# Kernel optimization log

Measured on AMD Instinct MI355X. Metric: run time of the kernel, lower is better.

## Reference

```python
import jax, jax.numpy as jnp
import numpy as np

NUM_HEADS = 12
DIM = 768


def _ste_sign(x):
    # forward: sign with sign(0) = +1; backward: pass-through on |x| <= 1
    s = jnp.where(x >= 0, 1.0, -1.0).astype(x.dtype)
    base = jnp.clip(x, -1.0, 1.0)
    return base + jax.lax.stop_gradient(s - base)


def _quantize_qk(x):
    # s = mean(|x|) over last two dims (differentiable), times STE sign
    s = jnp.mean(jnp.abs(x), axis=(-2, -1), keepdims=True)
    return s * _ste_sign(x)


def _round_ste(z):
    return z + jax.lax.stop_gradient(jnp.round(z) - z)


def _quantize_p(x):
    qmax = 255.0
    s = 1.0 / qmax
    q = jnp.clip(_round_ste(x / s), 0.0, qmax)
    return s * q


def _quantize_v(x):
    # SymQuantizer fwd: per-column (dim=-2) absmax, detached; 8-bit symmetric
    m = jax.lax.stop_gradient(jnp.max(jnp.abs(x), axis=-2, keepdims=True))
    s = 127.0 / (m + 1e-6)
    qz = jnp.round(x * s) / (s + 1e-6)
    # backward STE: pass-through where -2 < x < 2 (clip_val = [-2, 2])
    base = jnp.clip(x, -2.0, 2.0)
    return base + jax.lax.stop_gradient(qz - base)


def _attention(x, w_qkv, w_proj, b_proj):
    B, C, H, W = x.shape
    N = H * W
    nh = NUM_HEADS
    hd = C // nh
    scale = hd ** (-0.5)
    xf = x.reshape(B, C, N).transpose(0, 2, 1)          # [B, N, C]
    qkv = xf @ w_qkv.T                                   # [B, N, 3C]
    qkv = qkv.reshape(B, N, 3, nh, hd).transpose(2, 0, 3, 1, 4)  # [3, B, h, N, d]
    q, k, v = qkv[0], qkv[1], qkv[2]
    q = _quantize_qk(q)
    k = _quantize_qk(k)
    attn = jnp.einsum('bhnd,bhmd->bhnm', q, k) * scale   # [B, h, N, N]
    attn = jax.nn.softmax(attn, axis=-1)
    attn = _quantize_p(attn)
    v = _quantize_v(v)
    out = jnp.einsum('bhnm,bhmd->bhnd', attn, v)         # [B, h, N, d]
    out = out.transpose(0, 2, 1, 3).reshape(B, N, C)
    out = out @ w_proj.T + b_proj                        # [B, N, C]
    return out.transpose(0, 2, 1).reshape(B, C, H, W)


def setup_inputs() -> dict:
    key = jax.random.key(0)
    k1, k2, k3, k4 = jax.random.split(key, 4)
    B, C, H, W = 16, DIM, 24, 24
    x = jax.random.normal(k1, (B, C, H, W), dtype=jnp.float32)
    w_qkv = jax.random.normal(k2, (3 * C, C), dtype=jnp.float32) * 0.02
    w_proj = jax.random.normal(k3, (C, C), dtype=jnp.float32) * 0.02
    b_proj = jax.random.normal(k4, (C,), dtype=jnp.float32) * 0.02
    return {"x": x, "w_qkv": w_qkv, "w_proj": w_proj, "b_proj": b_proj}


def reference(x, w_qkv, w_proj, b_proj):
    return _attention(x, w_qkv, w_proj, b_proj)
```

## Files before the change

kernel.cpp:

```cpp
#include <hip/hip_runtime.h>
#include <hip/hip_bf16.h>

#define B_   16
#define NH   12
#define NTOK 576
#define HD   64
#define CH   768
#define NELEM (B_*NH*NTOK*HD)
#define VT8STRIDE (NTOK*HD*4)

typedef short v8s __attribute__((ext_vector_type(8)));
typedef short v4s __attribute__((ext_vector_type(4)));
typedef float v4f __attribute__((ext_vector_type(4)));
typedef int   v4i __attribute__((ext_vector_type(4)));

static __device__ __forceinline__ void split4(const float* f, v4s& hi, v4s& lo)
{
    #pragma unroll
    for (int i = 0; i < 4; ++i) {
        __hip_bfloat16 h = __float2bfloat16(f[i]);
        float hf = __bfloat162float(h);
        __hip_bfloat16 l = __float2bfloat16(f[i] - hf);
        hi[i] = __builtin_bit_cast(short, h);
        lo[i] = __builtin_bit_cast(short, l);
    }
}

__global__ __launch_bounds__(256) void qkv_mfma(const float* __restrict__ x,
    const float* __restrict__ w, float* __restrict__ q, float* __restrict__ k,
    float* __restrict__ v)
{
    __shared__ short Ah[64*40], Al[64*40];
    __shared__ short Bh[256*40], Bl[256*40];
    const int tid = threadIdx.x;
    int g = blockIdx.x;
    g = (g & 7) * 162 + (g >> 3);
    const int b  = g / 81;
    const int rr = g % 81;
    const int jb = rr / 9;
    const int mb = rr % 9;
    const int n0 = mb * 64;
    const int j0 = jb * 256;
    const int lane = tid & 63, wv = tid >> 6;

    const int cq  = tid & 7;
    const int rw0 = tid >> 3;

    const float* xb  = x + (size_t)b * CH * NTOK + n0;
    const float* wbp = w + (size_t)j0 * CH;

    float areg[2][4];
    float breg[8][4];

    #pragma unroll
    for (int s = 0; s < 2; ++s) {
        const int nl = rw0 + 32*s;
        #pragma unroll
        for (int i = 0; i < 4; ++i)
            areg[s][i] = xb[(size_t)(cq*4 + i) * NTOK + nl];
    }
    #pragma unroll
    for (int s = 0; s < 8; ++s) {
        const int jl = rw0 + 32*s;
        const float4 t = *(const float4*)(wbp + (size_t)jl * CH + cq*4);
        breg[s][0]=t.x; breg[s][1]=t.y; breg[s][2]=t.z; breg[s][3]=t.w;
    }

    v4f acc[4][4];
    #pragma unroll
    for (int a = 0; a < 4; ++a)
        #pragma unroll
        for (int c = 0; c < 4; ++c) acc[a][c] = (v4f){0.f,0.f,0.f,0.f};

    for (int it = 0; it < 24; ++it) {
        __syncthreads();
        #pragma unroll
        for (int s = 0; s < 2; ++s) {
            v4s hi, lo; split4(areg[s], hi, lo);
            const int nl = rw0 + 32*s;
            *(v4s*)&Ah[nl*40 + cq*4] = hi;
            *(v4s*)&Al[nl*40 + cq*4] = lo;
        }
        #pragma unroll
        for (int s = 0; s < 8; ++s) {
            v4s hi, lo; split4(breg[s], hi, lo);
            const int jl = rw0 + 32*s;
            *(v4s*)&Bh[jl*40 + cq*4] = hi;
            *(v4s*)&Bl[jl*40 + cq*4] = lo;
        }
        __syncthreads();
        if (it < 23) {
            const int c0 = (it + 1) * 32;
            #pragma unroll
            for (int s = 0; s < 2; ++s) {
                const int nl = rw0 + 32*s;
                #pragma unroll
                for (int i = 0; i < 4; ++i)
                    areg[s][i] = xb[(size_t)(c0 + cq*4 + i) * NTOK + nl];
            }
            #pragma unroll
            for (int s = 0; s < 8; ++s) {
                const int jl = rw0 + 32*s;
                const float4 t = *(const float4*)(wbp + (size_t)jl * CH + c0 + cq*4);
                breg[s][0]=t.x; breg[s][1]=t.y; breg[s][2]=t.z; breg[s][3]=t.w;
            }
        }
        const int krow = lane & 15;
        const int k0   = (lane >> 4) * 8;
        v8s ah[4], al2[4], bh[4], bl[4];
        #pragma unroll
        for (int mt = 0; mt < 4; ++mt) {
            ah[mt]  = *(v8s*)&Ah[(mt*16 + krow)*40 + k0];
            al2[mt] = *(v8s*)&Al[(mt*16 + krow)*40 + k0];
        }
        #pragma unroll
        for (int jt = 0; jt < 4; ++jt) {
            bh[jt] = *(v8s*)&Bh[(wv*64 + jt*16 + krow)*40 + k0];
            bl[jt] = *(v8s*)&Bl[(wv*64 + jt*16 + krow)*40 + k0];
        }
        #pragma unroll
        for (int mt = 0; mt < 4; ++mt)
            #pragma unroll
            for (int jt = 0; jt < 4; ++jt) {
                acc[mt][jt] = __builtin_amdgcn_mfma_f32_16x16x32_bf16(ah[mt],  bh[jt], acc[mt][jt], 0, 0, 0);
                acc[mt][jt] = __builtin_amdgcn_mfma_f32_16x16x32_bf16(ah[mt],  bl[jt], acc[mt][jt], 0, 0, 0);
                acc[mt][jt] = __builtin_amdgcn_mfma_f32_16x16x32_bf16(al2[mt], bh[jt], acc[mt][jt], 0, 0, 0);
            }
    }

    const int sec = jb / 3;
    float* dst = (sec == 0) ? q : (sec == 1) ? k : v;
    const int h    = (jb % 3) * 4 + wv;
    const int col  = lane & 15;
    const int row4 = (lane >> 4) * 4;
    #pragma unroll
    for (int mt = 0; mt < 4; ++mt)
        #pragma unroll
        for (int jt = 0; jt < 4; ++jt) {
            const int dd = jt*16 + col;
            float* o = dst + (((size_t)b*NH + h)*NTOK + n0 + mt*16 + row4) * HD + dd;
            #pragma unroll
            for (int rg = 0; rg < 4; ++rg)
                o[(size_t)rg * HD] = acc[mt][jt][rg];
        }
}

__global__ __launch_bounds__(256) void prep(const float* __restrict__ q,
    const float* __restrict__ k, const float* v,
    unsigned long long* __restrict__ qm, unsigned long long* __restrict__ km,
    float* __restrict__ cs, const float* __restrict__ x,
    const float* __restrict__ wqkv, unsigned char* vt8,
    int* __restrict__ colsum_g, float* __restrict__ scale_g)
{
    const int bh  = blockIdx.x;
    const int tid = threadIdx.x;
    const int b   = bh / NH;
    const int h   = bh % NH;
    const size_t base = (size_t)bh * (NTOK * HD);
    const float* qb = q + base;
    const float* kb = k + base;
    const float* vb = v + base;

    __shared__ float r1[256], r2[256], vm[256];
    __shared__ float svs[64];
    __shared__ unsigned qml32[2*NTOK], kml32[2*NTOK];
    __shared__ int fixq[512];
    __shared__ int fixn;
    __shared__ unsigned char vt[64*592];
    __shared__ int csum_s[256];
    if (tid == 0) fixn = 0;

    float sq = 0.f, sk = 0.f;
    for (int i = tid; i < NTOK * HD; i += 256) {
        sq += fabsf(qb[i]);
        sk += fabsf(kb[i]);
    }
    r1[tid] = sq; r2[tid] = sk;

    float m = 0.f;
    const int d = tid & 63;
    for (int n = tid >> 6; n < NTOK; n += 4)
        m = fmaxf(m, fabsf(vb[n * HD + d]));
    vm[tid] = m;
    __syncthreads();

    for (int s = 128; s > 0; s >>= 1) {
        if (tid < s) { r1[tid] += r1[tid + s]; r2[tid] += r2[tid + s]; }
        __syncthreads();
    }
    if (tid == 0) {
        const float msq = r1[0] * (1.f / (NTOK * HD));
        const float msk = r2[0] * (1.f / (NTOK * HD));
        cs[bh] = msq * msk * 0.125f;
    }
    if (tid < 64) {
        const float mm = fmaxf(fmaxf(vm[tid], vm[tid + 64]),
                               fmaxf(vm[tid + 128], vm[tid + 192]));
        svs[tid] = 127.f / (mm + 1e-6f);
    }
    __syncthreads();

    const int wv = tid >> 6, lane = tid & 63;
    for (int n = wv; n < NTOK; n += 4) {
        const float qv = qb[n * HD + lane];
        const float kv = kb[n * HD + lane];
        const unsigned long long mq = __ballot(qv >= 0.f);
        const unsigned long long mk = __ballot(kv >= 0.f);
        if (lane == 0) {
            qml32[2*n] = (unsigned)mq; qml32[2*n+1] = (unsigned)(mq >> 32);
            kml32[2*n] = (unsigned)mk; kml32[2*n+1] = (unsigned)(mk >> 32);
        }
        if (fabsf(qv) < 1e-4f) {
            int s_ = atomicAdd(&fixn, 1);
            if (s_ < 512) fixq[s_] = n | (lane << 10);
        }
        if (fabsf(kv) < 1e-4f) {
            int s_ = atomicAdd(&fixn, 1);
            if (s_ < 512) fixq[s_] = n | (lane << 10) | (1 << 16);
        }
    }

    for (int i = tid; i < NTOK * HD; i += 256) {
        const float s = svs[i & 63];
        const int iq = (int)rintf(vb[i] * s);
        vt[(i & 63) * 592 + (i >> 6)] = (unsigned char)(iq & 255);
    }
    __syncthreads();

    const int nf = min(fixn, 512);
    for (int e = tid; e < nf; e += 256) {
        const int rec = fixq[e];
        const int n   = rec & 1023;
        const int dd  = (rec >> 10) & 63;
        const int isk = (rec >> 16) & 1;
        const int row = isk * CH + h * HD + dd;
        const float* wr = wqkv + (size_t)row * CH;
        const float* xr = x + (size_t)b * CH * NTOK + n;
        float s = 0.f;
        #pragma unroll 8
        for (int c = 0; c < CH; ++c)
            s = fmaf(xr[(size_t)c * NTOK], wr[c], s);
        unsigned* arr = isk ? kml32 : qml32;
        const unsigned bit = 1u << (dd & 31);
        const int idx = 2*n + (dd >> 5);
        if (s >= 0.f) atomicOr(&arr[idx], bit);
        else          atomicAnd(&arr[idx], ~bit);
    }

    {
        int part = 0;
        for (int n = tid >> 6; n < NTOK; n += 4)
            part += (int)(signed char)vt[(tid & 63) * 592 + n];
        csum_s[tid] = part;
    }
    __syncthreads();

    for (int n = tid; n < NTOK; n += 256) {
        qm[(size_t)bh*NTOK + n] = (unsigned long long)qml32[2*n] |
                                  ((unsigned long long)qml32[2*n+1] << 32);
        km[(size_t)bh*NTOK + n] = (unsigned long long)kml32[2*n] |
                                  ((unsigned long long)kml32[2*n+1] << 32);
    }
    if (tid < 64) {
        colsum_g[bh*64 + tid] = csum_s[tid] + csum_s[tid+64] +
                                csum_s[tid+128] + csum_s[tid+192];
        scale_g[bh*64 + tid] = (1.f/255.f) / (svs[tid] + 1e-6f);
    }
    {
        unsigned char* dst = vt8 + (size_t)bh * VT8STRIDE;
        #pragma unroll
        for (int t = 0; t < 9; ++t) {
            const int idx = tid + t*256;
            const int row = idx / 36, seg = idx % 36;
            *(int4*)(dst + row*576 + seg*16) = *(const int4*)&vt[row*592 + seg*16];
        }
    }
}

__global__ __launch_bounds__(256) void attn_i8(
    const unsigned long long* __restrict__ qm,
    const unsigned long long* __restrict__ km,
    const unsigned char* __restrict__ vt8, const float* __restrict__ cs,
    const int* __restrict__ colsum_g, const float* __restrict__ scale_g,
    float* __restrict__ pre)
{
    const int tid = threadIdx.x;
    const int t0 = blockIdx.x << 6;
    const int h  = blockIdx.y;
    const int b  = blockIdx.z;
    const int bh = b * NH + h;

    __shared__ unsigned long long kml[NTOK];
    __shared__ unsigned long long qml[64];
    __shared__ float rs[64];
    __shared__ float table[65];
    __shared__ unsigned char vt[64*592];

    for (int i = tid; i < NTOK; i += 256) kml[i] = km[(size_t)bh * NTOK + i];
    if (tid < 64) qml[tid] = qm[(size_t)bh * NTOK + t0 + tid];
    const float c = cs[bh];
    if (tid < 65) table[tid] = __expf(c * (float)(64 - 2 * tid));
    {
        const unsigned char* src = vt8 + (size_t)bh * VT8STRIDE;
        #pragma unroll
        for (int t = 0; t < 9; ++t) {
            const int idx = tid + t*256;
            const int row = idx / 36, seg = idx % 36;
            *(int4*)&vt[row*592 + seg*16] = *(const int4*)(src + row*576 + seg*16);
        }
    }
    __syncthreads();

    const int wv = tid >> 6, lane = tid & 63;
    for (int r = wv; r < 64; r += 4) {
        const unsigned long long qq = qml[r];
        float s = 0.f;
        for (int m = lane; m < NTOK; m += 64) {
            const int pc = __popcll(qq ^ kml[m]);
            s += table[pc];
        }
        #pragma unroll
        for (int off = 32; off; off >>= 1) s += __shfl_xor(s, off, 64);
        if (lane == 0) rs[r] = 1.f / s;
    }
    __syncthreads();

    const int row_l = lane & 15;
    const int kgrp  = lane >> 4;
    const unsigned long long uq = qml[wv*16 + row_l];
    const float rsr = rs[wv*16 + row_l];
    v4i acc[4];
    #pragma unroll
    for (int jt = 0; jt < 4; ++jt) acc[jt] = (v4i){0,0,0,0};

    for (int ch = 0; ch < 9; ++ch) {
        const int mb = ch*64 + kgrp*16;
        int wds[4];
        #pragma unroll
        for (int wq = 0; wq < 4; ++wq) {
            int pk = 0;
            #pragma unroll
            for (int j = 0; j < 4; ++j) {
                const int pc = __popcll(uq ^ kml[mb + wq*4 + j]);
                const float p = table[pc] * rsr;
                const int iq = (int)rintf(p * 255.f) - 128;
                pk |= (iq & 255) << (8*j);
            }
            wds[wq] = pk;
        }
        v4i a; a[0]=wds[0]; a[1]=wds[1]; a[2]=wds[2]; a[3]=wds[3];
        #pragma unroll
        for (int jt = 0; jt < 4; ++jt) {
            const v4i bfr = *(const v4i*)&vt[(jt*16 + row_l)*592 + mb];
            acc[jt] = __builtin_amdgcn_mfma_i32_16x16x64_i8(a, bfr, acc[jt], 0, 0, 0);
        }
    }

    const int rb = kgrp * 4;
    #pragma unroll
    for (int jt = 0; jt < 4; ++jt) {
        const int dd = jt*16 + row_l;
        const int csd = colsum_g[bh*64 + dd];
        const float scd = scale_g[bh*64 + dd];
        #pragma unroll
        for (int rg = 0; rg < 4; ++rg) {
            const int n = t0 + wv*16 + rb + rg;
            pre[((size_t)b * NTOK + n) * CH + h * HD + dd] =
                (float)(acc[jt][rg] + 128 * csd) * scd;
        }
    }
}

__global__ __launch_bounds__(256) void proj_mfma(const float* __restrict__ pre,
    const float* __restrict__ w, const float* __restrict__ bias,
    float* __restrict__ out)
{
    __shared__ short Awh[256*40], Awl[256*40];
    __shared__ short Bph[64*40],  Bpl[64*40];
    const int tid = threadIdx.x;
    int g = blockIdx.x;
    g = (g & 7) * 54 + (g >> 3);
    const int b  = g / 27;
    const int rr = g % 27;
    const int cb = rr / 9;
    const int nb = rr % 9;
    const int co0 = cb * 256;
    const int nn0 = nb * 64;
    const int lane = tid & 63, wv = tid >> 6;
    const int cq  = tid & 7;
    const int rw0 = tid >> 3;

    const float* wp = w + (size_t)co0 * CH;
    const float* pb = pre + ((size_t)b * NTOK + nn0) * CH;

    float areg[8][4];
    float breg[2][4];

    #pragma unroll
    for (int s = 0; s < 8; ++s) {
        const int cl = rw0 + 32*s;
        const float4 t = *(const float4*)(wp + (size_t)cl * CH + cq*4);
        areg[s][0]=t.x; areg[s][1]=t.y; areg[s][2]=t.z; areg[s][3]=t.w;
    }
    #pragma unroll
    for (int s = 0; s < 2; ++s) {
        const int nl = rw0 + 32*s;
        const float4 t = *(const float4*)(pb + (size_t)nl * CH + cq*4);
        breg[s][0]=t.x; breg[s][1]=t.y; breg[s][2]=t.z; breg[s][3]=t.w;
    }

    v4f acc[4][4];
    #pragma unroll
    for (int a = 0; a < 4; ++a)
        #pragma unroll
        for (int c = 0; c < 4; ++c) acc[a][c] = (v4f){0.f,0.f,0.f,0.f};

    for (int it = 0; it < 24; ++it) {
        __syncthreads();
        #pragma unroll
        for (int s = 0; s < 8; ++s) {
            v4s hi, lo; split4(areg[s], hi, lo);
            const int cl = rw0 + 32*s;
            *(v4s*)&Awh[cl*40 + cq*4] = hi;
            *(v4s*)&Awl[cl*40 + cq*4] = lo;
        }
        #pragma unroll
        for (int s = 0; s < 2; ++s) {
            v4s hi, lo; split4(breg[s], hi, lo);
            const int nl = rw0 + 32*s;
            *(v4s*)&Bph[nl*40 + cq*4] = hi;
            *(v4s*)&Bpl[nl*40 + cq*4] = lo;
        }
        __syncthreads();
        if (it < 23) {
            const int k0g = (it + 1) * 32;
            #pragma unroll
            for (int s = 0; s < 8; ++s) {
                const int cl = rw0 + 32*s;
                const float4 t = *(const float4*)(wp + (size_t)cl * CH + k0g + cq*4);
                areg[s][0]=t.x; areg[s][1]=t.y; areg[s][2]=t.z; areg[s][3]=t.w;
            }
            #pragma unroll
            for (int s = 0; s < 2; ++s) {
                const int nl = rw0 + 32*s;
                const float4 t = *(const float4*)(pb + (size_t)nl * CH + k0g + cq*4);
                breg[s][0]=t.x; breg[s][1]=t.y; breg[s][2]=t.z; breg[s][3]=t.w;
            }
        }
        const int krow = lane & 15;
        const int k0   = (lane >> 4) * 8;
        v8s ah[4], al2[4], bh[4], bl[4];
        #pragma unroll
        for (int mt = 0; mt < 4; ++mt) {
            ah[mt]  = *(v8s*)&Awh[(wv*64 + mt*16 + krow)*40 + k0];
            al2[mt] = *(v8s*)&Awl[(wv*64 + mt*16 + krow)*40 + k0];
        }
        #pragma unroll
        for (int jt = 0; jt < 4; ++jt) {
            bh[jt] = *(v8s*)&Bph[(jt*16 + krow)*40 + k0];
            bl[jt] = *(v8s*)&Bpl[(jt*16 + krow)*40 + k0];
        }
        #pragma unroll
        for (int mt = 0; mt < 4; ++mt)
            #pragma unroll
            for (int jt = 0; jt < 4; ++jt) {
                acc[mt][jt] = __builtin_amdgcn_mfma_f32_16x16x32_bf16(ah[mt],  bh[jt], acc[mt][jt], 0, 0, 0);
                acc[mt][jt] = __builtin_amdgcn_mfma_f32_16x16x32_bf16(ah[mt],  bl[jt], acc[mt][jt], 0, 0, 0);
                acc[mt][jt] = __builtin_amdgcn_mfma_f32_16x16x32_bf16(al2[mt], bh[jt], acc[mt][jt], 0, 0, 0);
            }
    }

    const int col  = lane & 15;
    const int row4 = (lane >> 4) * 4;
    #pragma unroll
    for (int mt = 0; mt < 4; ++mt)
        #pragma unroll
        for (int rg = 0; rg < 4; ++rg) {
            const int co = co0 + wv*64 + mt*16 + row4 + rg;
            const float bi = bias[co];
            #pragma unroll
            for (int jt = 0; jt < 4; ++jt)
                out[((size_t)b * CH + co) * NTOK + nn0 + jt*16 + col] =
                    acc[mt][jt][rg] + bi;
        }
}

extern "C" void kernel_launch(void* const* d_in, const int* in_sizes, int n_in,
                              void* d_out, int out_size, void* d_ws, size_t ws_size,
                              hipStream_t stream)
{
    (void)in_sizes; (void)n_in; (void)out_size; (void)ws_size;
    const float* x     = (const float*)d_in[0];
    const float* wqkv  = (const float*)d_in[1];
    const float* wproj = (const float*)d_in[2];
    const float* bproj = (const float*)d_in[3];
    float* out = (float*)d_out;

    float* qbuf = (float*)d_ws;
    float* kbuf = qbuf + NELEM;
    float* vbuf = kbuf + NELEM;
    unsigned long long* qmask = (unsigned long long*)(vbuf + NELEM);
    unsigned long long* kmask = qmask + (B_ * NH * NTOK);
    float* cs = (float*)(kmask + (B_ * NH * NTOK));
    int*   colsum = (int*)(cs + B_ * NH);
    float* scale  = (float*)(colsum + B_ * NH * HD);
    unsigned char* vt8 = (unsigned char*)vbuf;

    qkv_mfma<<<dim3(1296), 256, 0, stream>>>(x, wqkv, qbuf, kbuf, vbuf);
    prep<<<dim3(B_ * NH), 256, 0, stream>>>(qbuf, kbuf, vbuf, qmask, kmask, cs,
                                            x, wqkv, vt8, colsum, scale);
    attn_i8<<<dim3(9, NH, B_), 256, 0, stream>>>(qmask, kmask, vt8, cs,
                                                 colsum, scale, qbuf);
    proj_mfma<<<dim3(432), 256, 0, stream>>>(qbuf, wproj, bproj, out);
}
```

Baseline: 504.0 us.

## Split prep kernel into chunked reduce, finalize, vquant and global fixup passes

Measured after the change: 574.3 us. 13.9% more time.

```diff
diff --git a/kernel.cpp b/kernel.cpp
--- a/kernel.cpp
+++ b/kernel.cpp
@@ -7,7 +7,9 @@
 #define HD   64
 #define CH   768
 #define NELEM (B_*NH*NTOK*HD)
-#define VT8STRIDE (NTOK*HD*4)
+#define VT8SZ (NTOK*HD)
+#define FIXCAP 16384
+#define VPAD 176
 
 typedef short v8s __attribute__((ext_vector_type(8)));
 typedef short v4s __attribute__((ext_vector_type(4)));
@@ -28,8 +30,10 @@
 
 __global__ __launch_bounds__(256) void qkv_mfma(const float* __restrict__ x,
     const float* __restrict__ w, float* __restrict__ q, float* __restrict__ k,
-    float* __restrict__ v)
-{
+    float* __restrict__ v, int* __restrict__ fixn_g)
+{
+    if (blockIdx.x == 0 && threadIdx.x == 0) *fixn_g = 0;
+
     __shared__ short Ah[64*40], Al[64*40];
     __shared__ short Bh[256*40], Bl[256*40];
     const int tid = threadIdx.x;
@@ -145,135 +149,130 @@
         }
 }
 
-__global__ __launch_bounds__(256) void prep(const float* __restrict__ q,
-    const float* __restrict__ k, const float* v,
+__global__ __launch_bounds__(256) void reduce_pass(
+    const float* __restrict__ q, const float* __restrict__ k,
+    const float* __restrict__ v,
     unsigned long long* __restrict__ qm, unsigned long long* __restrict__ km,
-    float* __restrict__ cs, const float* __restrict__ x,
-    const float* __restrict__ wqkv, unsigned char* vt8,
-    int* __restrict__ colsum_g, float* __restrict__ scale_g)
-{
-    const int bh  = blockIdx.x;
-    const int tid = threadIdx.x;
-    const int b   = bh / NH;
-    const int h   = bh % NH;
+    float* __restrict__ sumq_p, float* __restrict__ sumk_p,
+    float* __restrict__ vmax_p, int* __restrict__ fixq_g,
+    int* __restrict__ fixn_g)
+{
+    const int bh = blockIdx.x, ch = blockIdx.y;
+    const int tid = threadIdx.x, lane = tid & 63, wv = tid >> 6;
     const size_t base = (size_t)bh * (NTOK * HD);
     const float* qb = q + base;
     const float* kb = k + base;
     const float* vb = v + base;
+    const int n0 = ch * 144;
+
+    float sq = 0.f, sk = 0.f, vmx = 0.f;
+    for (int n = n0 + wv; n < n0 + 144; n += 4) {
+        const float qv = qb[n*HD + lane];
+        const float kv = kb[n*HD + lane];
+        const float vv = vb[n*HD + lane];
+        sq += fabsf(qv); sk += fabsf(kv); vmx = fmaxf(vmx, fabsf(vv));
+        const unsigned long long mq = __ballot(qv >= 0.f);
+        const unsigned long long mk = __ballot(kv >= 0.f);
+        if (lane == 0) {
+            qm[(size_t)bh*NTOK + n] = mq;
+            km[(size_t)bh*NTOK + n] = mk;
+        }
+        if (fabsf(qv) < 1e-4f) {
+            int s_ = atomicAdd(fixn_g, 1);
+            if (s_ < FIXCAP) fixq_g[s_] = bh | (n << 8) | (lane << 18);
+        }
+        if (fabsf(kv) < 1e-4f) {
+            int s_ = atomicAdd(fixn_g, 1);
+            if (s_ < FIXCAP) fixq_g[s_] = bh | (n << 8) | (lane << 18) | (1 << 24);
+        }
+    }
 
     __shared__ float r1[256], r2[256], vm[256];
-    __shared__ float svs[64];
-    __shared__ unsigned qml32[2*NTOK], kml32[2*NTOK];
-    __shared__ int fixq[512];
-    __shared__ int fixn;
-    __shared__ unsigned char vt[64*592];
-    __shared__ int csum_s[256];
-    if (tid == 0) fixn = 0;
-
-    float sq = 0.f, sk = 0.f;
-    for (int i = tid; i < NTOK * HD; i += 256) {
-        sq += fabsf(qb[i]);
-        sk += fabsf(kb[i]);
-    }
-    r1[tid] = sq; r2[tid] = sk;
-
-    float m = 0.f;
-    const int d = tid & 63;
-    for (int n = tid >> 6; n < NTOK; n += 4)
-        m = fmaxf(m, fabsf(vb[n * HD + d]));
-    vm[tid] = m;
+    r1[tid] = sq; r2[tid] = sk; vm[tid] = vmx;
     __syncthreads();
-
     for (int s = 128; s > 0; s >>= 1) {
         if (tid < s) { r1[tid] += r1[tid + s]; r2[tid] += r2[tid + s]; }
         __syncthreads();
     }
-    if (tid == 0) {
-        const float msq = r1[0] * (1.f / (NTOK * HD));
-        const float msk = r2[0] * (1.f / (NTOK * HD));
+    if (tid == 0) { sumq_p[bh*4 + ch] = r1[0]; sumk_p[bh*4 + ch] = r2[0]; }
+    if (tid < 64)
+        vmax_p[((size_t)bh*4 + ch)*64 + tid] =
+            fmaxf(fmaxf(vm[tid], vm[tid+64]), fmaxf(vm[tid+128], vm[tid+192]));
+}
+
+__global__ __launch_bounds__(64) void finalize(
+    const float* __restrict__ sumq_p, const float* __restrict__ sumk_p,
+    const float* __restrict__ vmax_p, float* __restrict__ cs,
+    float* __restrict__ svs_g, float* __restrict__ scale_g)
+{
+    const int bh = blockIdx.x, d = threadIdx.x;
+    if (d == 0) {
+        const float msq = (sumq_p[bh*4] + sumq_p[bh*4+1] + sumq_p[bh*4+2] +
+                           sumq_p[bh*4+3]) * (1.f / (NTOK * HD));
+        const float msk = (sumk_p[bh*4] + sumk_p[bh*4+1] + sumk_p[bh*4+2] +
+                           sumk_p[bh*4+3]) * (1.f / (NTOK * HD));
         cs[bh] = msq * msk * 0.125f;
     }
-    if (tid < 64) {
-        const float mm = fmaxf(fmaxf(vm[tid], vm[tid + 64]),
-                               fmaxf(vm[tid + 128], vm[tid + 192]));
-        svs[tid] = 127.f / (mm + 1e-6f);
-    }
+    const float mm = fmaxf(
+        fmaxf(vmax_p[((size_t)bh*4+0)*64 + d], vmax_p[((size_t)bh*4+1)*64 + d]),
+        fmaxf(vmax_p[((size_t)bh*4+2)*64 + d], vmax_p[((size_t)bh*4+3)*64 + d]));
+    const float svs = 127.f / (mm + 1e-6f);
+    svs_g[bh*64 + d] = svs;
+    scale_g[bh*64 + d] = (1.f/255.f) / (svs + 1e-6f);
+}
+
+__global__ __launch_bounds__(256) void vquant(const float* __restrict__ v,
+    const float* __restrict__ svs_g, unsigned char* __restrict__ vt8,
+    int* __restrict__ csum_p)
+{
+    const int bh = blockIdx.x, ch = blockIdx.y;
+    const int tid = threadIdx.x, d = tid & 63;
+    const float* vb = v + (size_t)bh * NTOK * HD + ch * 144 * HD;
+    __shared__ unsigned char vt[64 * VPAD];
+    __shared__ int cs_l[256];
+    const float s = svs_g[bh*64 + d];
+    int part = 0;
+    for (int i = tid; i < 144 * 64; i += 256) {
+        const int nl = i >> 6;
+        const int iq = (int)rintf(vb[i] * s);
+        part += iq;
+        vt[d*VPAD + nl] = (unsigned char)(iq & 255);
+    }
+    cs_l[tid] = part;
     __syncthreads();
-
-    const int wv = tid >> 6, lane = tid & 63;
-    for (int n = wv; n < NTOK; n += 4) {
-        const float qv = qb[n * HD + lane];
-        const float kv = kb[n * HD + lane];
-        const unsigned long long mq = __ballot(qv >= 0.f);
-        const unsigned long long mk = __ballot(kv >= 0.f);
-        if (lane == 0) {
-            qml32[2*n] = (unsigned)mq; qml32[2*n+1] = (unsigned)(mq >> 32);
-            kml32[2*n] = (unsigned)mk; kml32[2*n+1] = (unsigned)(mk >> 32);
-        }
-        if (fabsf(qv) < 1e-4f) {
-            int s_ = atomicAdd(&fixn, 1);
-            if (s_ < 512) fixq[s_] = n | (lane << 10);
-        }
-        if (fabsf(kv) < 1e-4f) {
-            int s_ = atomicAdd(&fixn, 1);
-            if (s_ < 512) fixq[s_] = n | (lane << 10) | (1 << 16);
-        }
-    }
-
-    for (int i = tid; i < NTOK * HD; i += 256) {
-        const float s = svs[i & 63];
-        const int iq = (int)rintf(vb[i] * s);
-        vt[(i & 63) * 592 + (i >> 6)] = (unsigned char)(iq & 255);
-    }
-    __syncthreads();
-
-    const int nf = min(fixn, 512);
-    for (int e = tid; e < nf; e += 256) {
-        const int rec = fixq[e];
-        const int n   = rec & 1023;
-        const int dd  = (rec >> 10) & 63;
-        const int isk = (rec >> 16) & 1;
-        const int row = isk * CH + h * HD + dd;
-        const float* wr = wqkv + (size_t)row * CH;
+    if (tid < 64)
+        csum_p[((size_t)bh*4 + ch)*64 + tid] =
+            cs_l[tid] + cs_l[tid+64] + cs_l[tid+128] + cs_l[tid+192];
+    unsigned char* dst = vt8 + (size_t)bh * VT8SZ + ch * 144;
+    for (int idx = tid; idx < 576; idx += 256) {
+        const int row = idx / 9, seg = idx % 9;
+        *(int4*)(dst + row*576 + seg*16) = *(const int4*)&vt[row*VPAD + seg*16];
+    }
+}
+
+__global__ __launch_bounds__(256) void fixup(const float* __restrict__ x,
+    const float* __restrict__ wqkv, unsigned long long* __restrict__ qm,
+    unsigned long long* __restrict__ km, const int* __restrict__ fixq_g,
+    const int* __restrict__ fixn_g)
+{
+    const int total = min(*fixn_g, FIXCAP);
+    for (int e = blockIdx.x*256 + threadIdx.x; e < total; e += gridDim.x*256) {
+        const int rec = fixq_g[e];
+        const int bh  = rec & 255;
+        const int n   = (rec >> 8) & 1023;
+        const int dd  = (rec >> 18) & 63;
+        const int isk = (rec >> 24) & 1;
+        const int b = bh / NH, h = bh % NH;
+        const float* wr = wqkv + (size_t)(isk*CH + h*HD + dd) * CH;
         const float* xr = x + (size_t)b * CH * NTOK + n;
         float s = 0.f;
         #pragma unroll 8
         for (int c = 0; c < CH; ++c)
             s = fmaf(xr[(size_t)c * NTOK], wr[c], s);
-        unsigned* arr = isk ? kml32 : qml32;
+        unsigned* a32 = (unsigned*)((isk ? km : qm) + (size_t)bh*NTOK + n);
         const unsigned bit = 1u << (dd & 31);
-        const int idx = 2*n + (dd >> 5);
-        if (s >= 0.f) atomicOr(&arr[idx], bit);
-        else          atomicAnd(&arr[idx], ~bit);
-    }
-
-    {
-        int part = 0;
-        for (int n = tid >> 6; n < NTOK; n += 4)
-            part += (int)(signed char)vt[(tid & 63) * 592 + n];
-        csum_s[tid] = part;
-    }
-    __syncthreads();
-
-    for (int n = tid; n < NTOK; n += 256) {
-        qm[(size_t)bh*NTOK + n] = (unsigned long long)qml32[2*n] |
-                                  ((unsigned long long)qml32[2*n+1] << 32);
-        km[(size_t)bh*NTOK + n] = (unsigned long long)kml32[2*n] |
-                                  ((unsigned long long)kml32[2*n+1] << 32);
-    }
-    if (tid < 64) {
-        colsum_g[bh*64 + tid] = csum_s[tid] + csum_s[tid+64] +
-                                csum_s[tid+128] + csum_s[tid+192];
-        scale_g[bh*64 + tid] = (1.f/255.f) / (svs[tid] + 1e-6f);
-    }
-    {
-        unsigned char* dst = vt8 + (size_t)bh * VT8STRIDE;
-        #pragma unroll
-        for (int t = 0; t < 9; ++t) {
-            const int idx = tid + t*256;
-            const int row = idx / 36, seg = idx % 36;
-            *(int4*)(dst + row*576 + seg*16) = *(const int4*)&vt[row*592 + seg*16];
-        }
+        if (s >= 0.f) atomicOr(&a32[dd >> 5], bit);
+        else          atomicAnd(&a32[dd >> 5], ~bit);
     }
 }
 
@@ -281,7 +280,7 @@
     const unsigned long long* __restrict__ qm,
     const unsigned long long* __restrict__ km,
     const unsigned char* __restrict__ vt8, const float* __restrict__ cs,
-    const int* __restrict__ colsum_g, const float* __restrict__ scale_g,
+    const int* __restrict__ csum_p, const float* __restrict__ scale_g,
     float* __restrict__ pre)
 {
     const int tid = threadIdx.x;
@@ -301,7 +300,7 @@
     const float c = cs[bh];
     if (tid < 65) table[tid] = __expf(c * (float)(64 - 2 * tid));
     {
-        const unsigned char* src = vt8 + (size_t)bh * VT8STRIDE;
+        const unsigned char* src = vt8 + (size_t)bh * VT8SZ;
         #pragma unroll
         for (int t = 0; t < 9; ++t) {
             const int idx = tid + t*256;
@@ -360,7 +359,10 @@
     #pragma unroll
     for (int jt = 0; jt < 4; ++jt) {
         const int dd = jt*16 + row_l;
-        const int csd = colsum_g[bh*64 + dd];
+        const int csd = csum_p[((size_t)bh*4+0)*64 + dd] +
+                        csum_p[((size_t)bh*4+1)*64 + dd] +
+                        csum_p[((size_t)bh*4+2)*64 + dd] +
+                        csum_p[((size_t)bh*4+3)*64 + dd];
         const float scd = scale_g[bh*64 + dd];
         #pragma unroll
         for (int rg = 0; rg < 4; ++rg) {
@@ -501,15 +503,25 @@
     float* vbuf = kbuf + NELEM;
     unsigned long long* qmask = (unsigned long long*)(vbuf + NELEM);
     unsigned long long* kmask = qmask + (B_ * NH * NTOK);
-    float* cs = (float*)(kmask + (B_ * NH * NTOK));
-    int*   colsum = (int*)(cs + B_ * NH);
-    float* scale  = (float*)(colsum + B_ * NH * HD);
-    unsigned char* vt8 = (unsigned char*)vbuf;
-
-    qkv_mfma<<<dim3(1296), 256, 0, stream>>>(x, wqkv, qbuf, kbuf, vbuf);
-    prep<<<dim3(B_ * NH), 256, 0, stream>>>(qbuf, kbuf, vbuf, qmask, kmask, cs,
-                                            x, wqkv, vt8, colsum, scale);
+    float* cs     = (float*)(kmask + (B_ * NH * NTOK));
+    int*   csum_p = (int*)(cs + B_ * NH);
+    float* scale  = (float*)(csum_p + B_ * NH * 4 * HD);
+    float* svs_g  = scale + B_ * NH * HD;
+    float* sumq_p = svs_g + B_ * NH * HD;
+    float* sumk_p = sumq_p + B_ * NH * 4;
+    float* vmax_p = sumk_p + B_ * NH * 4;
+    int*   fixq_g = (int*)(vmax_p + B_ * NH * 4 * HD);
+    int*   fixn_g = fixq_g + FIXCAP;
+    unsigned char* vt8 = (unsigned char*)kbuf;
+
+    qkv_mfma<<<dim3(1296), 256, 0, stream>>>(x, wqkv, qbuf, kbuf, vbuf, fixn_g);
+    reduce_pass<<<dim3(B_*NH, 4), 256, 0, stream>>>(qbuf, kbuf, vbuf,
+        qmask, kmask, sumq_p, sumk_p, vmax_p, fixq_g, fixn_g);
+    finalize<<<dim3(B_*NH), 64, 0, stream>>>(sumq_p, sumk_p, vmax_p,
+        cs, svs_g, scale);
+    vquant<<<dim3(B_*NH, 4), 256, 0, stream>>>(vbuf, svs_g, vt8, csum_p);
+    fixup<<<dim3(32), 256, 0, stream>>>(x, wqkv, qmask, kmask, fixq_g, fixn_g);
     attn_i8<<<dim3(9, NH, B_), 256, 0, stream>>>(qmask, kmask, vt8, cs,
-                                                 colsum, scale, qbuf);
+                                                 csum_p, scale, qbuf);
     proj_mfma<<<dim3(432), 256, 0, stream>>>(qbuf, wproj, bproj, out);
 }
```
